# Performance work log

Hardware: AMD Instinct MI355X
Metric: run time of the kernel (lower is better)

Reference implementation:

```python
import jax, jax.numpy as jnp
import numpy as np

N, E, L = 10000, 160000, 4
IN, HID, HEADS, OUT = 15, 128, 4, 5
C = HID              # per-head out_channels of TransformerConv
HC = HEADS * C       # concatenated width = 512
EPS = 1e-5


def _w(k, shape, fan_in):
    return (jax.random.normal(k, shape, jnp.float32) / np.sqrt(fan_in)).astype(jnp.float32)


def setup_inputs() -> dict:
    key = jax.random.key(0)
    ks = jax.random.split(key, 24)
    return {
        "x": jax.random.normal(ks[0], (N, IN), jnp.float32),
        "edge_index": jax.random.randint(ks[1], (2, E), 0, N, dtype=jnp.int32),
        # input / output projections
        "W_in": _w(ks[2], (IN, HID), IN), "b_in": jnp.zeros((HID,), jnp.float32),
        "W_out": _w(ks[3], (HID, OUT), HID), "b_out": jnp.zeros((OUT,), jnp.float32),
        # stacked per-layer TransformerConv params (L leading dim)
        "Wq": _w(ks[4], (L, HID, HC), HID), "bq": jnp.zeros((L, HC), jnp.float32),
        "Wk": _w(ks[5], (L, HID, HC), HID), "bk": jnp.zeros((L, HC), jnp.float32),
        "Wv": _w(ks[6], (L, HID, HC), HID), "bv": jnp.zeros((L, HC), jnp.float32),
        "Wskip": _w(ks[7], (L, HID, HC), HID), "bskip": jnp.zeros((L, HC), jnp.float32),
        "Wbeta": _w(ks[8], (L, 3 * HC, 1), 3 * HC),
        "ln_w": jnp.ones((L, HC), jnp.float32), "ln_b": jnp.zeros((L, HC), jnp.float32),
        "Wproj": _w(ks[9], (L, HC, HID), HC), "bproj": jnp.zeros((L, HID), jnp.float32),
    }


def _forward(x, edge_index, W_in, b_in, Wq, bq, Wk, bk, Wv, bv,
             Wskip, bskip, Wbeta, ln_w, ln_b, Wproj, bproj, W_out, b_out):
    src, dst = edge_index[0], edge_index[1]  # message j->i aggregated at dst
    h = x @ W_in + b_in  # [N, HID]

    def layer(h, p):
        Wq_, bq_, Wk_, bk_, Wv_, bv_, Ws_, bs_, Wb_, lw, lb, Wp_, bp_ = p
        q = (h @ Wq_ + bq_).reshape(N, HEADS, C)
        k = (h @ Wk_ + bk_).reshape(N, HEADS, C)
        v = (h @ Wv_ + bv_).reshape(N, HEADS, C)
        # attention logits per edge/head: [E, HEADS]
        logits = (q[dst] * k[src]).sum(-1) / jnp.sqrt(jnp.float32(C))
        # segment softmax over incoming edges of each target node
        m = jax.ops.segment_max(logits, dst, num_segments=N)
        ex = jnp.exp(logits - m[dst])
        den = jax.ops.segment_sum(ex, dst, num_segments=N)
        alpha = ex / (den[dst] + 1e-16)
        out = jax.ops.segment_sum(v[src] * alpha[..., None], dst,
                                  num_segments=N).reshape(N, HC)
        # beta-gated skip (TransformerConv beta=True)
        skip = h @ Ws_ + bs_
        beta = jax.nn.sigmoid(jnp.concatenate([out, skip, out - skip], -1) @ Wb_)  # [N,1]
        out = beta * skip + (1.0 - beta) * out
        # PyG LayerNorm, mode='graph' (single graph): normalize over all elements
        xc = out - out.mean()
        out = xc / (jnp.sqrt((xc * xc).mean()) + EPS) * lw + lb
        out = out @ Wp_ + bp_
        return jax.nn.relu(out + h), None

    params = (Wq, bq, Wk, bk, Wv, bv, Wskip, bskip, Wbeta, ln_w, ln_b, Wproj, bproj)
    h, _ = jax.lax.scan(layer, h, params)
    return h @ W_out + b_out


def reference(x, edge_index, W_in, b_in, Wq, bq, Wk, bk, Wv, bv,
              Wskip, bskip, Wbeta, ln_w, ln_b, Wproj, bproj, W_out, b_out):
    return _forward(x, edge_index, W_in, b_in, Wq, bq, Wk, bk, Wv, bv,
                    Wskip, bskip, Wbeta, ln_w, ln_b, Wproj, bproj, W_out, b_out)
```

## Files before the change

kernel.cpp:

```cpp
#include <hip/hip_runtime.h>
#include <math.h>

#define NN 10000
#define NE 160000
#define HCW 512
#define CH 128
#define NLAYERS 4
#define LN_EPS 1e-5f
#define NBUCK 128

typedef short bf16x8 __attribute__((ext_vector_type(8)));
typedef float f32x4 __attribute__((ext_vector_type(4)));

__device__ inline unsigned short f2bf(float f) {
    union { float f; unsigned int u; } x; x.f = f;
    unsigned int u = x.u;
    return (unsigned short)((u + 0x7FFFu + ((u >> 16) & 1u)) >> 16);
}
__device__ inline float bf2f(unsigned short s) {
    union { unsigned int u; float f; } x; x.u = ((unsigned int)s) << 16;
    return x.f;
}
__device__ inline float lo16(unsigned int u) {
    union { unsigned int x; float f; } v; v.x = u << 16; return v.f;
}
__device__ inline float hi16(unsigned int u) {
    union { unsigned int x; float f; } v; v.x = u & 0xffff0000u; return v.f;
}

template<int CTRL>
__device__ inline float dppadd(float x) {
    int y = __builtin_amdgcn_update_dpp(0, __float_as_int(x), CTRL, 0xF, 0xF, true);
    return x + __int_as_float(y);
}
__device__ inline float red16(float x) {
    x = dppadd<0x128>(x);
    x = dppadd<0x124>(x);
    x = dppadd<0x122>(x);
    x = dppadd<0x121>(x);
    return x;
}
__device__ inline float red64(float x) {
    x = red16(x);
    x += __shfl_xor(x, 16, 64);
    x += __shfl_xor(x, 32, 64);
    return x;
}

__device__ inline float dot8(const float4& q0, const float4& q1, const uint4& kk) {
    return q0.x * lo16(kk.x) + q0.y * hi16(kk.x)
         + q0.z * lo16(kk.y) + q0.w * hi16(kk.y)
         + q1.x * lo16(kk.z) + q1.y * hi16(kk.z)
         + q1.z * lo16(kk.w) + q1.w * hi16(kk.w);
}

__global__ void k_init(int* cnt, int* fill, float* stats) {
    int i = blockIdx.x * blockDim.x + threadIdx.x;
    if (i < NN) { cnt[i] = 0; fill[i] = 0; }
    if (i < NLAYERS * NBUCK * 16) stats[i] = 0.f;
}

__global__ void k_count(const int* __restrict__ dst, int* __restrict__ cnt) {
    int e = blockIdx.x * blockDim.x + threadIdx.x;
    if (e < NE) atomicAdd(&cnt[dst[e]], 1);
}

__global__ __launch_bounds__(1024) void k_scan(const int* __restrict__ cnt, int* __restrict__ offs) {
    __shared__ int sh[1024];
    __shared__ int carry;
    if (threadIdx.x == 0) carry = 0;
    __syncthreads();
    for (int base = 0; base < NN; base += 1024) {
        int i = base + threadIdx.x;
        int v = (i < NN) ? cnt[i] : 0;
        sh[threadIdx.x] = v;
        __syncthreads();
        for (int off = 1; off < 1024; off <<= 1) {
            int t = (threadIdx.x >= off) ? sh[threadIdx.x - off] : 0;
            __syncthreads();
            sh[threadIdx.x] += t;
            __syncthreads();
        }
        int incl = sh[threadIdx.x];
        if (i < NN) offs[i] = carry + incl - v;
        __syncthreads();
        if (threadIdx.x == 1023) carry += sh[1023];
        __syncthreads();
    }
    if (threadIdx.x == 0) offs[NN] = carry;
}

__global__ void k_fill(const int* __restrict__ src, const int* __restrict__ dst,
                       const int* __restrict__ offs, int* __restrict__ fill,
                       int* __restrict__ col) {
    int e = blockIdx.x * blockDim.x + threadIdx.x;
    if (e < NE) {
        int d = dst[e];
        int p = offs[d] + atomicAdd(&fill[d], 1);
        col[p] = src[e];
    }
}

__global__ void k_wconv(const float* __restrict__ Wq, const float* __restrict__ Wk,
                        const float* __restrict__ Wv, const float* __restrict__ Ws,
                        const float* __restrict__ Wp,
                        unsigned short* __restrict__ wt_qkvs,
                        unsigned short* __restrict__ wpt) {
    int id = blockIdx.x * blockDim.x + threadIdx.x;
    if (id < NLAYERS * 2048 * 128) {
        int l = id >> 18;
        int rem = id & 262143;
        int n = rem >> 7, k = rem & 127;
        int mat = n >> 9, wcol = n & 511;
        const float* W = (mat == 0) ? Wq : (mat == 1) ? Wk : (mat == 2) ? Wv : Ws;
        wt_qkvs[id] = f2bf(W[(size_t)l * 65536 + k * 512 + wcol]);
    } else if (id < NLAYERS * 2048 * 128 + NLAYERS * 128 * 512) {
        int id2 = id - NLAYERS * 2048 * 128;
        int l = id2 >> 16;
        int rem = id2 & 65535;
        int n = rem >> 9, k = rem & 511;
        wpt[(size_t)l * 65536 + n * 512 + k] = f2bf(Wp[(size_t)l * 65536 + k * 128 + n]);
    }
}

__global__ __launch_bounds__(128) void k_inproj(const float* __restrict__ x,
                                                const float* __restrict__ W,
                                                const float* __restrict__ b,
                                                float* __restrict__ h,
                                                unsigned short* __restrict__ h_bf) {
    int n = blockIdx.x;
    int j = threadIdx.x;
    float acc = b[j];
#pragma unroll
    for (int i = 0; i < 15; i++) acc += x[n * 15 + i] * W[i * 128 + j];
    h[n * 128 + j] = acc;
    h_bf[n * 128 + j] = f2bf(acc);
}

__global__ __launch_bounds__(256) void k_qkvs_mfma(
    const unsigned short* __restrict__ h_bf,
    const unsigned short* __restrict__ Wt,
    const float* __restrict__ bq, const float* __restrict__ bk,
    const float* __restrict__ bv, const float* __restrict__ bs,
    unsigned short* __restrict__ qb16, unsigned short* __restrict__ kv16,
    unsigned short* __restrict__ sb16) {
    __shared__ unsigned short As[128 * 128];
    __shared__ unsigned short Bs[128 * 128];
    int row0 = blockIdx.x * 128;
    int n0 = blockIdx.y * 128;
    int t = threadIdx.x;
#pragma unroll
    for (int i = 0; i < 8; i++) {
        int c = t + i * 256;
        int r = c >> 4, cc = c & 15;
        int gr = row0 + r;
        uint4 v = make_uint4(0, 0, 0, 0);
        if (gr < NN) v = *(const uint4*)(h_bf + (size_t)gr * 128 + cc * 8);
        int sc = (r << 4) | (cc ^ (r & 7));
        *(uint4*)(As + sc * 8) = v;
    }
#pragma unroll
    for (int i = 0; i < 8; i++) {
        int c = t + i * 256;
        int r = c >> 4, cc = c & 15;
        uint4 v = *(const uint4*)(Wt + (size_t)(n0 + r) * 128 + cc * 8);
        int sc = (r << 4) | (cc ^ (r & 7));
        *(uint4*)(Bs + sc * 8) = v;
    }
    __syncthreads();
    int wave = t >> 6, lane = t & 63;
    int wr = (wave >> 1) * 64, wc = (wave & 1) * 64;
    int lr = lane & 15, lk = lane >> 4;
    f32x4 acc[4][4] = {};
#pragma unroll
    for (int ks = 0; ks < 4; ks++) {
        bf16x8 a[4], b[4];
#pragma unroll
        for (int mi = 0; mi < 4; mi++) {
            int r = wr + mi * 16 + lr;
            int cc = (ks * 4 + lk) ^ (r & 7);
            a[mi] = *(const bf16x8*)(As + (((r << 4) | cc) * 8));
        }
#pragma unroll
        for (int ni = 0; ni < 4; ni++) {
            int r = wc + ni * 16 + lr;
            int cc = (ks * 4 + lk) ^ (r & 7);
            b[ni] = *(const bf16x8*)(Bs + (((r << 4) | cc) * 8));
        }
#pragma unroll
        for (int mi = 0; mi < 4; mi++)
#pragma unroll
            for (int ni = 0; ni < 4; ni++)
                acc[mi][ni] = __builtin_amdgcn_mfma_f32_16x16x32_bf16(a[mi], b[ni], acc[mi][ni], 0, 0, 0);
    }
    int mat = blockIdx.y >> 2;
    int wcol0 = n0 & 511;
    const float* bias_p = (mat == 0) ? bq : (mat == 1) ? bk : (mat == 2) ? bv : bs;
    __syncthreads();
#pragma unroll
    for (int ni = 0; ni < 4; ni++) {
        int colL = wc + ni * 16 + lr;
        float bias = bias_p[wcol0 + colL];
#pragma unroll
        for (int mi = 0; mi < 4; mi++) {
            int rowB = wr + mi * 16 + 4 * lk;
#pragma unroll
            for (int r = 0; r < 4; r++) {
                int row = rowB + r;
                unsigned int w = (unsigned int)(row * 64 + (colL >> 1));
                w ^= ((row >> 2) & 7) << 3;
                As[w * 2 + (colL & 1)] = f2bf(acc[mi][ni][r] + bias);
            }
        }
    }
    __syncthreads();
    unsigned short* outp = (mat == 0) ? qb16 : (mat == 3) ? sb16 : kv16;
    int rowStride = (mat == 1 || mat == 2) ? 1024 : 512;
    int cbase = wcol0 + ((mat == 2) ? 512 : 0);
#pragma unroll
    for (int i = 0; i < 8; i++) {
        int idx = t + i * 256;
        int row2 = idx >> 4;
        int c8 = (idx & 15) * 8;
        int gr = row0 + row2;
        if (gr < NN) {
            unsigned int wb = (unsigned int)(row2 * 64 + (idx & 15) * 4);
            wb ^= ((row2 >> 2) & 7) << 3;
            uint4 v = *(const uint4*)(As + wb * 2);
            *(uint4*)(outp + (size_t)gr * rowStride + cbase + c8) = v;
        }
    }
}

__global__ __launch_bounds__(256) void k_attn_beta(
    const unsigned short* __restrict__ qb16,
    const unsigned short* __restrict__ kv16,
    const unsigned short* __restrict__ sb16,
    const float* __restrict__ Wb,
    const int* __restrict__ offs, const int* __restrict__ col,
    unsigned short* __restrict__ gated16, float* __restrict__ stats) {
    int wave = threadIdx.x >> 6;
    int lane = threadIdx.x & 63;
    int n = blockIdx.x * 4 + wave;
    const int off = ((lane >> 4) << 7) + ((lane & 15) << 3);
    uint4 qq = *(const uint4*)(qb16 + (size_t)n * HCW + off);
    float4 q0 = {lo16(qq.x), hi16(qq.x), lo16(qq.y), hi16(qq.y)};
    float4 q1 = {lo16(qq.z), hi16(qq.z), lo16(qq.w), hi16(qq.w)};
    int beg = offs[n], end = offs[n + 1];
    const float scale = 0.08838834764831845f;

    float m[4], s[4];
    float4 a0[4], a1[4];
#pragma unroll
    for (int i = 0; i < 4; i++) {
        m[i] = -INFINITY; s[i] = 0.f;
        a0[i] = make_float4(0.f, 0.f, 0.f, 0.f);
        a1[i] = make_float4(0.f, 0.f, 0.f, 0.f);
    }

    for (int p = beg; p < end; p += 4) {
        uint4 kk[4], vv[4];
        bool has[4];
#pragma unroll
        for (int i = 0; i < 4; i++) {
            int pi = p + i;
            has[i] = (pi < end);
            int sn = col[has[i] ? pi : p];
            const unsigned short* bp_ = kv16 + ((size_t)sn << 10) + off;
            kk[i] = *(const uint4*)bp_;
            vv[i] = *(const uint4*)(bp_ + 512);
        }
#pragma unroll
        for (int i = 0; i < 4; i++) {
            if (!has[i]) continue;
            float l = red16(dot8(q0, q1, kk[i])) * scale;
            if (l <= m[i] + 8.f) {
                float w = __expf(l - m[i]);
                s[i] += w;
                a0[i].x += w * lo16(vv[i].x); a0[i].y += w * hi16(vv[i].x);
                a0[i].z += w * lo16(vv[i].y); a0[i].w += w * hi16(vv[i].y);
                a1[i].x += w * lo16(vv[i].z); a1[i].y += w * hi16(vv[i].z);
                a1[i].z += w * lo16(vv[i].w); a1[i].w += w * hi16(vv[i].w);
            } else {
                float sc = __expf(m[i] - l);
                s[i] = s[i] * sc + 1.f;
                a0[i].x = a0[i].x * sc + lo16(vv[i].x); a0[i].y = a0[i].y * sc + hi16(vv[i].x);
                a0[i].z = a0[i].z * sc + lo16(vv[i].y); a0[i].w = a0[i].w * sc + hi16(vv[i].y);
                a1[i].x = a1[i].x * sc + lo16(vv[i].z); a1[i].y = a1[i].y * sc + hi16(vv[i].z);
                a1[i].z = a1[i].z * sc + lo16(vv[i].w); a1[i].w = a1[i].w * sc + hi16(vv[i].w);
                m[i] = l;
            }
        }
    }
#pragma unroll
    for (int i = 1; i < 4; i++) {
        float mn = fmaxf(m[0], m[i]);
        float c1 = (s[0] > 0.f) ? __expf(m[0] - mn) : 0.f;
        float c2 = (s[i] > 0.f) ? __expf(m[i] - mn) : 0.f;
        s[0] = s[0] * c1 + s[i] * c2;
        a0[0].x = a0[0].x * c1 + a0[i].x * c2; a0[0].y = a0[0].y * c1 + a0[i].y * c2;
        a0[0].z = a0[0].z * c1 + a0[i].z * c2; a0[0].w = a0[0].w * c1 + a0[i].w * c2;
        a1[0].x = a1[0].x * c1 + a1[i].x * c2; a1[0].y = a1[0].y * c1 + a1[i].y * c2;
        a1[0].z = a1[0].z * c1 + a1[i].z * c2; a1[0].w = a1[0].w * c1 + a1[i].w * c2;
        m[0] = mn;
    }
    float inv = (s[0] > 0.f) ? 1.f / s[0] : 0.f;
    float o[8] = {a0[0].x * inv, a0[0].y * inv, a0[0].z * inv, a0[0].w * inv,
                  a1[0].x * inv, a1[0].y * inv, a1[0].z * inv, a1[0].w * inv};

    uint4 sku = *(const uint4*)(sb16 + (size_t)n * HCW + off);
    float sk[8] = {lo16(sku.x), hi16(sku.x), lo16(sku.y), hi16(sku.y),
                   lo16(sku.z), hi16(sku.z), lo16(sku.w), hi16(sku.w)};

    float part = 0.f;
#pragma unroll
    for (int j = 0; j < 8; j++) {
        int c = off + j;
        part += o[j] * Wb[c] + sk[j] * Wb[512 + c] + (o[j] - sk[j]) * Wb[1024 + c];
    }
    part = red64(part);
    float beta = 1.f / (1.f + __expf(-part));

    unsigned int gu[4];
    float ls = 0.f, lq = 0.f;
#pragma unroll
    for (int j = 0; j < 4; j++) {
        float gx = beta * sk[2 * j] + (1.f - beta) * o[2 * j];
        float gy = beta * sk[2 * j + 1] + (1.f - beta) * o[2 * j + 1];
        gu[j] = (unsigned int)f2bf(gx) | ((unsigned int)f2bf(gy) << 16);
        float gxr = lo16(gu[j]), gyr = hi16(gu[j]);
        ls += gxr + gyr;
        lq += gxr * gxr + gyr * gyr;
    }
    *(uint4*)(gated16 + (size_t)n * HCW + off) = *(uint4*)gu;

    ls = red64(ls);
    lq = red64(lq);
    __shared__ float r2[8];
    if (lane == 0) { r2[wave] = ls; r2[4 + wave] = lq; }
    __syncthreads();
    if (threadIdx.x == 0) {
        int b = blockIdx.x & (NBUCK - 1);
        atomicAdd(&stats[b * 16], r2[0] + r2[1] + r2[2] + r2[3]);
        atomicAdd(&stats[b * 16 + 1], r2[4] + r2[5] + r2[6] + r2[7]);
    }
}

__global__ __launch_bounds__(512) void k_proj_mfma(
    const unsigned short* __restrict__ gated16,
    const unsigned short* __restrict__ Wpt,
    const float* __restrict__ bp,
    const float* __restrict__ lw, const float* __restrict__ lb,
    const float* __restrict__ stats,
    float* __restrict__ h, unsigned short* __restrict__ h_bf) {
    __shared__ unsigned short As[64 * 128];
    __shared__ unsigned short Bs[128 * 128];
    int row0 = blockIdx.x * 64;
    int t = threadIdx.x;
    float ssum = 0.f, sq = 0.f;
#pragma unroll 16
    for (int i = 0; i < NBUCK; i++) { ssum += stats[i * 16]; sq += stats[i * 16 + 1]; }
    const float invM = 1.f / (NN * 512.f);
    float mean = ssum * invM;
    float ms = sq * invM - mean * mean;
    float rstd = 1.f / (sqrtf(fmaxf(ms, 0.f)) + LN_EPS);
    int wave = t >> 6, lane = t & 63;
    int wr = (wave >> 1) * 16, wc = (wave & 1) * 64;
    int lr = lane & 15, lk = lane >> 4;
    f32x4 acc[4] = {};
    for (int kc = 0; kc < 4; kc++) {
        __syncthreads();
#pragma unroll
        for (int i = 0; i < 2; i++) {
            int c = t + i * 512;
            int r = c >> 4, cc = c & 15;
            int gr = row0 + r;
            int gk = kc * 128 + cc * 8;
            unsigned short u[8];
            if (gr < NN) {
                uint4 gv = *(const uint4*)(gated16 + (size_t)gr * 512 + gk);
                float vals[8] = {lo16(gv.x), hi16(gv.x), lo16(gv.y), hi16(gv.y),
                                 lo16(gv.z), hi16(gv.z), lo16(gv.w), hi16(gv.w)};
#pragma unroll
                for (int j = 0; j < 8; j++)
                    u[j] = f2bf((vals[j] - mean) * rstd * lw[gk + j] + lb[gk + j]);
            } else {
#pragma unroll
                for (int j = 0; j < 8; j++) u[j] = 0;
            }
            int sc = (r << 4) | (cc ^ (r & 7));
            *(uint4*)(As + sc * 8) = *(uint4*)u;
        }
#pragma unroll
        for (int i = 0; i < 4; i++) {
            int c = t + i * 512;
            int r = c >> 4, cc = c & 15;
            uint4 v = *(const uint4*)(Wpt + (size_t)r * 512 + kc * 128 + cc * 8);
            int sc = (r << 4) | (cc ^ (r & 7));
            *(uint4*)(Bs + sc * 8) = v;
        }
        __syncthreads();
#pragma unroll
        for (int ks = 0; ks < 4; ks++) {
            bf16x8 a, b[4];
            {
                int r = wr + lr;
                int cc = (ks * 4 + lk) ^ (r & 7);
                a = *(const bf16x8*)(As + (((r << 4) | cc) * 8));
            }
#pragma unroll
            for (int ni = 0; ni < 4; ni++) {
                int r = wc + ni * 16 + lr;
                int cc = (ks * 4 + lk) ^ (r & 7);
                b[ni] = *(const bf16x8*)(Bs + (((r << 4) | cc) * 8));
            }
#pragma unroll
            for (int ni = 0; ni < 4; ni++)
                acc[ni] = __builtin_amdgcn_mfma_f32_16x16x32_bf16(a, b[ni], acc[ni], 0, 0, 0);
        }
    }
#pragma unroll
    for (int ni = 0; ni < 4; ni++) {
        int gc = wc + ni * 16 + lr;
        float bias = bp[gc];
        int gr0 = row0 + wr + 4 * lk;
#pragma unroll
        for (int r = 0; r < 4; r++) {
            int grr = gr0 + r;
            if (grr < NN) {
                float o = acc[ni][r] + bias + h[(size_t)grr * 128 + gc];
                o = fmaxf(o, 0.f);
                h[(size_t)grr * 128 + gc] = o;
                h_bf[(size_t)grr * 128 + gc] = f2bf(o);
            }
        }
    }
}

__global__ void k_out(const float* __restrict__ h, const float* __restrict__ W,
                      const float* __restrict__ b, float* __restrict__ out) {
    int i = blockIdx.x * blockDim.x + threadIdx.x;
    if (i >= NN * 5) return;
    int n = i / 5, j = i % 5;
    float acc = b[j];
    for (int k = 0; k < 128; k++) acc += h[(size_t)n * 128 + k] * W[k * 5 + j];
    out[i] = acc;
}

extern "C" void kernel_launch(void* const* d_in, const int* in_sizes, int n_in,
                              void* d_out, int out_size, void* d_ws, size_t ws_size,
                              hipStream_t stream) {
    const float* x     = (const float*)d_in[0];
    const int* ei      = (const int*)d_in[1];
    const float* W_in  = (const float*)d_in[2];
    const float* b_in  = (const float*)d_in[3];
    const float* W_out = (const float*)d_in[4];
    const float* b_out = (const float*)d_in[5];
    const float* Wq    = (const float*)d_in[6];
    const float* bq    = (const float*)d_in[7];
    const float* Wk    = (const float*)d_in[8];
    const float* bk    = (const float*)d_in[9];
    const float* Wv    = (const float*)d_in[10];
    const float* bv    = (const float*)d_in[11];
    const float* Wsk   = (const float*)d_in[12];
    const float* bsk   = (const float*)d_in[13];
    const float* Wbeta = (const float*)d_in[14];
    const float* ln_w  = (const float*)d_in[15];
    const float* ln_b  = (const float*)d_in[16];
    const float* Wproj = (const float*)d_in[17];
    const float* bproj = (const float*)d_in[18];
    float* out = (float*)d_out;

    float* h     = (float*)d_ws;
    float* stats = h + (size_t)NN * 128;
    int* offs = (int*)(stats + NLAYERS * NBUCK * 16);
    int* cnt  = offs + (NN + 1);
    int* fill = cnt + NN;
    int* col  = fill + NN;
    unsigned short* h_bf = (unsigned short*)(((uintptr_t)(col + NE) + 15) & ~(uintptr_t)15);
    unsigned short* qb16 = h_bf + (size_t)NN * 128;
    unsigned short* sb16 = qb16 + (size_t)NN * 512;
    unsigned short* kv16 = sb16 + (size_t)NN * 512;
    unsigned short* wt_qkvs = kv16 + (size_t)NN * 1024;
    unsigned short* wpt = wt_qkvs + (size_t)NLAYERS * 2048 * 128;
    unsigned short* gated16 = qb16;

    const int* src = ei;
    const int* dst = ei + NE;

    k_init<<<(NN + 255) / 256, 256, 0, stream>>>(cnt, fill, stats);
    k_count<<<(NE + 255) / 256, 256, 0, stream>>>(dst, cnt);
    k_scan<<<1, 1024, 0, stream>>>(cnt, offs);
    k_fill<<<(NE + 255) / 256, 256, 0, stream>>>(src, dst, offs, fill, col);
    {
        int tot = NLAYERS * 2048 * 128 + NLAYERS * 128 * 512;
        k_wconv<<<(tot + 255) / 256, 256, 0, stream>>>(Wq, Wk, Wv, Wsk, Wproj, wt_qkvs, wpt);
    }
    k_inproj<<<NN, 128, 0, stream>>>(x, W_in, b_in, h, h_bf);

    for (int l = 0; l < NLAYERS; ++l) {
        const unsigned short* Wt_ = wt_qkvs + (size_t)l * 2048 * 128;
        const unsigned short* Wp_ = wpt + (size_t)l * 128 * 512;
        const float* bq_ = bq + l * 512;
        const float* bk_ = bk + l * 512;
        const float* bv_ = bv + l * 512;
        const float* bs_ = bsk + l * 512;
        const float* Wb_ = Wbeta + (size_t)l * 1536;
        const float* lw_ = ln_w + l * 512;
        const float* lb_ = ln_b + l * 512;
        const float* bp_ = bproj + l * 128;
        float* st = stats + (size_t)l * NBUCK * 16;

        dim3 g1((NN + 127) / 128, 16);
        k_qkvs_mfma<<<g1, 256, 0, stream>>>(h_bf, Wt_, bq_, bk_, bv_, bs_,
                                            qb16, kv16, sb16);
        k_attn_beta<<<NN / 4, 256, 0, stream>>>(qb16, kv16, sb16, Wb_, offs, col, gated16, st);
        k_proj_mfma<<<(NN + 63) / 64, 512, 0, stream>>>(gated16, Wp_, bp_, lw_, lb_, st, h, h_bf);
    }
    k_out<<<(NN * 5 + 255) / 256, 256, 0, stream>>>(h, W_out, b_out, out);
}
```

Before: 448.8 us.

## Split each node's edge loop across four waves and merge softmax state in LDS

After: 446.4 us. About the same (-0.5%).

```diff
diff --git a/kernel.cpp b/kernel.cpp
--- a/kernel.cpp
+++ b/kernel.cpp
@@ -239,10 +239,11 @@
     const float* __restrict__ Wb,
     const int* __restrict__ offs, const int* __restrict__ col,
     unsigned short* __restrict__ gated16, float* __restrict__ stats) {
+    int n = blockIdx.x;
     int wave = threadIdx.x >> 6;
     int lane = threadIdx.x & 63;
-    int n = blockIdx.x * 4 + wave;
-    const int off = ((lane >> 4) << 7) + ((lane & 15) << 3);
+    int head = lane >> 4;
+    const int off = (head << 7) + ((lane & 15) << 3);
     uint4 qq = *(const uint4*)(qb16 + (size_t)n * HCW + off);
     float4 q0 = {lo16(qq.x), hi16(qq.x), lo16(qq.y), hi16(qq.y)};
     float4 q1 = {lo16(qq.z), hi16(qq.z), lo16(qq.w), hi16(qq.w)};
@@ -258,12 +259,12 @@
         a1[i] = make_float4(0.f, 0.f, 0.f, 0.f);
     }
 
-    for (int p = beg; p < end; p += 4) {
+    for (int p = beg + wave; p < end; p += 16) {
         uint4 kk[4], vv[4];
         bool has[4];
 #pragma unroll
         for (int i = 0; i < 4; i++) {
-            int pi = p + i;
+            int pi = p + i * 4;
             has[i] = (pi < end);
             int sn = col[has[i] ? pi : p];
             const unsigned short* bp_ = kv16 + ((size_t)sn << 10) + off;
@@ -304,9 +305,36 @@
         a1[0].z = a1[0].z * c1 + a1[i].z * c2; a1[0].w = a1[0].w * c1 + a1[i].w * c2;
         m[0] = mn;
     }
-    float inv = (s[0] > 0.f) ? 1.f / s[0] : 0.f;
-    float o[8] = {a0[0].x * inv, a0[0].y * inv, a0[0].z * inv, a0[0].w * inv,
-                  a1[0].x * inv, a1[0].y * inv, a1[0].z * inv, a1[0].w * inv};
+
+    __shared__ float lds_acc[4][512];
+    __shared__ float lds_m[4][4], lds_s[4][4];
+    *(float4*)&lds_acc[wave][off] = a0[0];
+    *(float4*)&lds_acc[wave][off + 4] = a1[0];
+    if ((lane & 15) == 0) { lds_m[wave][head] = m[0]; lds_s[wave][head] = s[0]; }
+    __syncthreads();
+    if (wave != 0) return;
+
+    float M = -INFINITY, S = 0.f;
+    float4 A0 = {0.f, 0.f, 0.f, 0.f}, A1 = {0.f, 0.f, 0.f, 0.f};
+#pragma unroll
+    for (int w = 0; w < 4; w++) {
+        float mw = lds_m[w][head];
+        float sw = lds_s[w][head];
+        float4 b0 = *(const float4*)&lds_acc[w][off];
+        float4 b1 = *(const float4*)&lds_acc[w][off + 4];
+        float mn = fmaxf(M, mw);
+        float c1 = (S > 0.f) ? __expf(M - mn) : 0.f;
+        float c2 = (sw > 0.f) ? __expf(mw - mn) : 0.f;
+        S = S * c1 + sw * c2;
+        A0.x = A0.x * c1 + b0.x * c2; A0.y = A0.y * c1 + b0.y * c2;
+        A0.z = A0.z * c1 + b0.z * c2; A0.w = A0.w * c1 + b0.w * c2;
+        A1.x = A1.x * c1 + b1.x * c2; A1.y = A1.y * c1 + b1.y * c2;
+        A1.z = A1.z * c1 + b1.z * c2; A1.w = A1.w * c1 + b1.w * c2;
+        M = mn;
+    }
+    float inv = (S > 0.f) ? 1.f / S : 0.f;
+    float o[8] = {A0.x * inv, A0.y * inv, A0.z * inv, A0.w * inv,
+                  A1.x * inv, A1.y * inv, A1.z * inv, A1.w * inv};
 
     uint4 sku = *(const uint4*)(sb16 + (size_t)n * HCW + off);
     float sk[8] = {lo16(sku.x), hi16(sku.x), lo16(sku.y), hi16(sku.y),
@@ -336,13 +364,10 @@
 
     ls = red64(ls);
     lq = red64(lq);
-    __shared__ float r2[8];
-    if (lane == 0) { r2[wave] = ls; r2[4 + wave] = lq; }
-    __syncthreads();
-    if (threadIdx.x == 0) {
-        int b = blockIdx.x & (NBUCK - 1);
-        atomicAdd(&stats[b * 16], r2[0] + r2[1] + r2[2] + r2[3]);
-        atomicAdd(&stats[b * 16 + 1], r2[4] + r2[5] + r2[6] + r2[7]);
+    if (lane == 0) {
+        int b = n & (NBUCK - 1);
+        atomicAdd(&stats[b * 16], ls);
+        atomicAdd(&stats[b * 16 + 1], lq);
     }
 }
 
@@ -437,14 +462,27 @@
     }
 }
 
-__global__ void k_out(const float* __restrict__ h, const float* __restrict__ W,
-                      const float* __restrict__ b, float* __restrict__ out) {
-    int i = blockIdx.x * blockDim.x + threadIdx.x;
-    if (i >= NN * 5) return;
-    int n = i / 5, j = i % 5;
-    float acc = b[j];
-    for (int k = 0; k < 128; k++) acc += h[(size_t)n * 128 + k] * W[k * 5 + j];
-    out[i] = acc;
+__global__ __launch_bounds__(256) void k_out(const float* __restrict__ h,
+                                             const float* __restrict__ W,
+                                             const float* __restrict__ b,
+                                             float* __restrict__ out) {
+    int wave = threadIdx.x >> 6, lane = threadIdx.x & 63;
+    int n = blockIdx.x * 4 + wave;
+    float2 hv = *(const float2*)(h + (size_t)n * 128 + lane * 2);
+    const float* w0 = W + (lane * 2) * 5;
+    float p0 = hv.x * w0[0] + hv.y * w0[5];
+    float p1 = hv.x * w0[1] + hv.y * w0[6];
+    float p2 = hv.x * w0[2] + hv.y * w0[7];
+    float p3 = hv.x * w0[3] + hv.y * w0[8];
+    float p4 = hv.x * w0[4] + hv.y * w0[9];
+    p0 = red64(p0); p1 = red64(p1); p2 = red64(p2); p3 = red64(p3); p4 = red64(p4);
+    if (lane == 0) {
+        out[n * 5 + 0] = p0 + b[0];
+        out[n * 5 + 1] = p1 + b[1];
+        out[n * 5 + 2] = p2 + b[2];
+        out[n * 5 + 3] = p3 + b[3];
+        out[n * 5 + 4] = p4 + b[4];
+    }
 }
 
 extern "C" void kernel_launch(void* const* d_in, const int* in_sizes, int n_in,
@@ -514,8 +552,8 @@
         dim3 g1((NN + 127) / 128, 16);
         k_qkvs_mfma<<<g1, 256, 0, stream>>>(h_bf, Wt_, bq_, bk_, bv_, bs_,
                                             qb16, kv16, sb16);
-        k_attn_beta<<<NN / 4, 256, 0, stream>>>(qb16, kv16, sb16, Wb_, offs, col, gated16, st);
+        k_attn_beta<<<NN, 256, 0, stream>>>(qb16, kv16, sb16, Wb_, offs, col, gated16, st);
         k_proj_mfma<<<(NN + 63) / 64, 512, 0, stream>>>(gated16, Wp_, bp_, lw_, lb_, st, h, h_bf);
     }
-    k_out<<<(NN * 5 + 255) / 256, 256, 0, stream>>>(h, W_out, b_out, out);
-}
+    k_out<<<NN / 4, 256, 0, stream>>>(h, W_out, b_out, out);
+}
```
